# Kernel tuning notes

Hardware: AMD Instinct MI355X
Metric: run time of the kernel (lower is better)

## Reference

```python
import jax, jax.numpy as jnp
import numpy as np

N_QUBITS = 10
N_LAYERS = 4
DIM = 1 << N_QUBITS            # 1024
N3 = 3 * N_QUBITS              # params per rotation layer
N_PARAM = N3 * (N_LAYERS + 1)  # 150
BATCH = 8192

_C64 = jnp.complex64


def _rx(t):
    c = jnp.cos(t / 2).astype(_C64)
    s = jnp.sin(t / 2).astype(_C64)
    return jnp.stack([jnp.stack([c, -1j * s]), jnp.stack([-1j * s, c])])


def _ry(t):
    c = jnp.cos(t / 2).astype(_C64)
    s = jnp.sin(t / 2).astype(_C64)
    return jnp.stack([jnp.stack([c, -s]), jnp.stack([s, c])])


def _rz(t):
    e = jnp.exp(-1j * t.astype(_C64) / 2)
    z = jnp.zeros((), _C64)
    return jnp.stack([jnp.stack([e, z]), jnp.stack([z, jnp.conj(e)])])


def _apply1(state, gate, wire):
    """Apply a 2x2 gate to qubit `wire` of state [B, 2, ..., 2]."""
    axis = wire + 1  # axis 0 is batch
    s = jnp.moveaxis(state, axis, -1)
    s = jnp.einsum('ij,...j->...i', gate, s)
    return jnp.moveaxis(s, -1, axis)


def _cnot(state, ctrl, tgt):
    a, b = ctrl + 1, tgt + 1
    s = jnp.moveaxis(state, (a, b), (-2, -1))  # [..., ctrl, tgt]
    s = jnp.stack([s[..., 0, :], s[..., 1, ::-1]], axis=-2)
    return jnp.moveaxis(s, (-2, -1), (a, b))


def setup_inputs() -> dict:
    key = jax.random.key(0)
    k1, k2 = jax.random.split(key)
    x = jax.random.normal(k1, (BATCH, DIM), dtype=jnp.float32)
    he_std = (2.0 ** 0.5) * (5.0 ** -0.5)  # gain * 5^-0.5, w_mul with lrmul=1
    weight = jax.random.uniform(k2, (N_PARAM,), minval=0.0,
                                maxval=2.0 * np.pi, dtype=jnp.float32) * he_std
    return {"x": x, "weight": weight}


def reference(x, weight):
    # encoding layer: L2-normalize then cast to complex amplitudes
    norm = jnp.linalg.norm(x, axis=-1, keepdims=True)
    s = (x / jnp.maximum(norm, 1e-12)).astype(_C64)
    s = s.reshape((x.shape[0],) + (2,) * N_QUBITS)

    for l in range(N_LAYERS):
        w = weight[l * N3:(l + 1) * N3]
        # XYZ layer: Rx, then Ry, then Rz on every qubit
        for q in range(N_QUBITS):
            s = _apply1(s, _rx(w[q]), q)
        for q in range(N_QUBITS):
            s = _apply1(s, _ry(w[N_QUBITS + q]), q)
        for q in range(N_QUBITS):
            s = _apply1(s, _rz(w[2 * N_QUBITS + q]), q)
        # ring of CNOTs
        for q in range(N_QUBITS):
            s = _cnot(s, q, (q + 1) % N_QUBITS)

    # final YZY layer
    w = weight[N_LAYERS * N3:]
    for q in range(N_QUBITS):
        s = _apply1(s, _ry(w[q]), q)
    for q in range(N_QUBITS):
        s = _apply1(s, _rz(w[N_QUBITS + q]), q)
    for q in range(N_QUBITS):
        s = _apply1(s, _ry(w[2 * N_QUBITS + q]), q)

    return s.reshape(x.shape[0], 1, DIM).real
```

## Files before the change

### kernel.cpp

```cpp
#include <hip/hip_runtime.h>
#include <stdint.h>

typedef uint16_t u16;
typedef __attribute__((ext_vector_type(2))) float f32x2;
typedef __attribute__((ext_vector_type(4))) float f32x4;
typedef __attribute__((ext_vector_type(8))) short short8;
typedef __attribute__((ext_vector_type(4))) float float4v;
typedef __attribute__((ext_vector_type(4))) uint16_t u16x4;
typedef __attribute__((ext_vector_type(8))) uint16_t u16x8;

#define DIMQ 1024
#define BATCH 8192
#define KDIM 1024
#define NDIM 1024

#define RDL(v, l) __int_as_float(__builtin_amdgcn_readlane(__float_as_int(v), (l)))

__device__ __forceinline__ u16 f2bf(float f) {
  uint32_t u = __float_as_uint(f);
  u += 0x7fffu + ((u >> 16) & 1u);
  return (u16)(u >> 16);
}

template<int MASK>
__device__ __forceinline__ float lane_xor(float x) {
  if constexpr (MASK == 1)
    return __int_as_float(__builtin_amdgcn_update_dpp(0, __float_as_int(x), 0xB1, 0xF, 0xF, true));
  else if constexpr (MASK == 2)
    return __int_as_float(__builtin_amdgcn_update_dpp(0, __float_as_int(x), 0x4E, 0xF, 0xF, true));
  else if constexpr (MASK == 8)
    return __int_as_float(__builtin_amdgcn_update_dpp(0, __float_as_int(x), 0x128, 0xF, 0xF, true));
  else if constexpr (MASK == 4)
    return __int_as_float(__builtin_amdgcn_ds_swizzle(__float_as_int(x), 0x101F));
  else if constexpr (MASK == 16)
    return __int_as_float(__builtin_amdgcn_ds_swizzle(__float_as_int(x), 0x401F));
  else
    return __shfl_xor(x, 32, 64);
}

template<int MASK>
__device__ __forceinline__ void lane_gate8(float* ar, float* ai, int lane,
    float u00r, float u00i, float u01r, float u01i,
    float u10r, float u10i, float u11r, float u11i) {
  bool hi = (lane & MASK) != 0;
  float cmr = hi ? u11r : u00r, cmi = hi ? u11i : u00i;
  float cor = hi ? u10r : u01r, coi = hi ? u10i : u01i;
  float otr[8], oti[8];
#pragma unroll
  for (int r = 0; r < 8; ++r) otr[r] = lane_xor<MASK>(ar[r]);
#pragma unroll
  for (int r = 0; r < 8; ++r) oti[r] = lane_xor<MASK>(ai[r]);
#pragma unroll
  for (int k = 0; k < 4; ++k) {
    f32x2 A = {ar[2*k], ar[2*k+1]}, I = {ai[2*k], ai[2*k+1]};
    f32x2 R = {otr[2*k], otr[2*k+1]}, J = {oti[2*k], oti[2*k+1]};
    f32x2 nr = A*cmr - I*cmi + R*cor - J*coi;
    f32x2 ni = I*cmr + A*cmi + J*cor + R*coi;
    ar[2*k] = nr[0]; ar[2*k+1] = nr[1];
    ai[2*k] = ni[0]; ai[2*k+1] = ni[1];
  }
}

__device__ __forceinline__ void bfly2(f32x2 &a0r, f32x2 &a0i, f32x2 &a1r, f32x2 &a1i,
    float u00r, float u00i, float u01r, float u01i,
    float u10r, float u10i, float u11r, float u11i) {
  f32x2 t0r = a0r*u00r - a0i*u00i + a1r*u01r - a1i*u01i;
  f32x2 t0i = a0i*u00r + a0r*u00i + a1i*u01r + a1r*u01i;
  f32x2 t1r = a0r*u10r - a0i*u10i + a1r*u11r - a1i*u11i;
  f32x2 t1i = a0i*u10r + a0r*u10i + a1i*u11r + a1r*u11i;
  a0r = t0r; a0i = t0i; a1r = t1r; a1i = t1i;
}

__device__ inline void cmul2x2(float* O, const float* A, const float* B) {
  for (int r = 0; r < 2; ++r)
    for (int c = 0; c < 2; ++c) {
      float re = 0.f, im = 0.f;
      for (int j = 0; j < 2; ++j) {
        float ar = A[(r*2+j)*2], ai = A[(r*2+j)*2+1];
        float br = B[(j*2+c)*2], bi = B[(j*2+c)*2+1];
        re += ar*br - ai*bi;
        im += ar*bi + ai*br;
      }
      O[(r*2+c)*2]   = re;
      O[(r*2+c)*2+1] = im;
    }
}
__device__ inline void mk_rx(float* m, float t) {
  float s, c; sincosf(0.5f*t, &s, &c);
  m[0]=c; m[1]=0; m[2]=0; m[3]=-s; m[4]=0; m[5]=-s; m[6]=c; m[7]=0;
}
__device__ inline void mk_ry(float* m, float t) {
  float s, c; sincosf(0.5f*t, &s, &c);
  m[0]=c; m[1]=0; m[2]=-s; m[3]=0; m[4]=s; m[5]=0; m[6]=c; m[7]=0;
}
__device__ inline void mk_rz(float* m, float t) {
  float s, c; sincosf(0.5f*t, &s, &c);
  m[0]=c; m[1]=-s; m[2]=0; m[3]=0; m[4]=0; m[5]=0; m[6]=c; m[7]=s;
}

__device__ __forceinline__ int padi(int y) { return y + (y >> 4); }

__device__ __forceinline__ void do_stage(int gbase, float (&ar)[8], float (&ai)[8],
    f32x2* __restrict__ slab,
    const int (&idP0)[8], const int (&idP1)[8],
    int wbase, int lane, int h,
    float O0, float O1, float O2, float O3,
    float O4, float O5, float O6, float O7) {
  __syncthreads();
#pragma unroll
  for (int j = 0; j < 8; ++j) slab[wbase + j] = (f32x2){ar[j], ai[j]};
  __syncthreads();
  {
    int g = gbase + 6;
    float c0r = h ? RDL(O4,g) : RDL(O0,g), c0i = h ? RDL(O5,g) : RDL(O1,g);
    float c1r = h ? RDL(O6,g) : RDL(O2,g), c1i = h ? RDL(O7,g) : RDL(O3,g);
    f32x2 v0[8], v1[8];
#pragma unroll
    for (int j = 0; j < 8; ++j) {
      v0[j] = slab[idP0[j]];
      v1[j] = slab[idP1[j]];
    }
#pragma unroll
    for (int k = 0; k < 4; ++k) {
      f32x2 Vr0 = {v0[2*k][0], v0[2*k+1][0]}, Vi0 = {v0[2*k][1], v0[2*k+1][1]};
      f32x2 Vr1 = {v1[2*k][0], v1[2*k+1][0]}, Vi1 = {v1[2*k][1], v1[2*k+1][1]};
      f32x2 nr = Vr0*c0r - Vi0*c0i + Vr1*c1r - Vi1*c1i;
      f32x2 ni = Vi0*c0r + Vr0*c0i + Vi1*c1r + Vr1*c1i;
      ar[2*k] = nr[0]; ar[2*k+1] = nr[1];
      ai[2*k] = ni[0]; ai[2*k+1] = ni[1];
    }
  }
  { int g = gbase + 7;
    float u0r=RDL(O0,g),u0i=RDL(O1,g),u1r=RDL(O2,g),u1i=RDL(O3,g);
    float u2r=RDL(O4,g),u2i=RDL(O5,g),u3r=RDL(O6,g),u3i=RDL(O7,g);
    f32x2 a0r={ar[0],ar[1]}, a0i={ai[0],ai[1]}, a1r={ar[4],ar[5]}, a1i={ai[4],ai[5]};
    bfly2(a0r,a0i,a1r,a1i, u0r,u0i,u1r,u1i,u2r,u2i,u3r,u3i);
    ar[0]=a0r[0];ar[1]=a0r[1];ai[0]=a0i[0];ai[1]=a0i[1];
    ar[4]=a1r[0];ar[5]=a1r[1];ai[4]=a1i[0];ai[5]=a1i[1];
    f32x2 b0r={ar[2],ar[3]}, b0i={ai[2],ai[3]}, b1r={ar[6],ar[7]}, b1i={ai[6],ai[7]};
    bfly2(b0r,b0i,b1r,b1i, u0r,u0i,u1r,u1i,u2r,u2i,u3r,u3i);
    ar[2]=b0r[0];ar[3]=b0r[1];ai[2]=b0i[0];ai[3]=b0i[1];
    ar[6]=b1r[0];ar[7]=b1r[1];ai[6]=b1i[0];ai[7]=b1i[1];
  }
  { int g = gbase + 8;
    float u0r=RDL(O0,g),u0i=RDL(O1,g),u1r=RDL(O2,g),u1i=RDL(O3,g);
    float u2r=RDL(O4,g),u2i=RDL(O5,g),u3r=RDL(O6,g),u3i=RDL(O7,g);
    f32x2 a0r={ar[0],ar[1]}, a0i={ai[0],ai[1]}, a1r={ar[2],ar[3]}, a1i={ai[2],ai[3]};
    bfly2(a0r,a0i,a1r,a1i, u0r,u0i,u1r,u1i,u2r,u2i,u3r,u3i);
    ar[0]=a0r[0];ar[1]=a0r[1];ai[0]=a0i[0];ai[1]=a0i[1];
    ar[2]=a1r[0];ar[3]=a1r[1];ai[2]=a1i[0];ai[3]=a1i[1];
    f32x2 b0r={ar[4],ar[5]}, b0i={ai[4],ai[5]}, b1r={ar[6],ar[7]}, b1i={ai[6],ai[7]};
    bfly2(b0r,b0i,b1r,b1i, u0r,u0i,u1r,u1i,u2r,u2i,u3r,u3i);
    ar[4]=b0r[0];ar[5]=b0r[1];ai[4]=b0i[0];ai[5]=b0i[1];
    ar[6]=b1r[0];ar[7]=b1r[1];ai[6]=b1i[0];ai[7]=b1i[1];
  }
  { int g = gbase + 9;
    float u0r=RDL(O0,g),u0i=RDL(O1,g),u1r=RDL(O2,g),u1i=RDL(O3,g);
    float u2r=RDL(O4,g),u2i=RDL(O5,g),u3r=RDL(O6,g),u3i=RDL(O7,g);
    f32x2 a0r={ar[0],ar[2]}, a0i={ai[0],ai[2]}, a1r={ar[1],ar[3]}, a1i={ai[1],ai[3]};
    bfly2(a0r,a0i,a1r,a1i, u0r,u0i,u1r,u1i,u2r,u2i,u3r,u3i);
    ar[0]=a0r[0];ar[2]=a0r[1];ai[0]=a0i[0];ai[2]=a0i[1];
    ar[1]=a1r[0];ar[3]=a1r[1];ai[1]=a1i[0];ai[3]=a1i[1];
    f32x2 b0r={ar[4],ar[6]}, b0i={ai[4],ai[6]}, b1r={ar[5],ar[7]}, b1i={ai[5],ai[7]};
    bfly2(b0r,b0i,b1r,b1i, u0r,u0i,u1r,u1i,u2r,u2i,u3r,u3i);
    ar[4]=b0r[0];ar[6]=b0r[1];ai[4]=b0i[0];ai[6]=b0i[1];
    ar[5]=b1r[0];ar[7]=b1r[1];ai[5]=b1i[0];ai[7]=b1i[1];
  }
  { int g = gbase + 0; lane_gate8<32>(ar, ai, lane, RDL(O0,g),RDL(O1,g),RDL(O2,g),RDL(O3,g),RDL(O4,g),RDL(O5,g),RDL(O6,g),RDL(O7,g)); }
  { int g = gbase + 1; lane_gate8<16>(ar, ai, lane, RDL(O0,g),RDL(O1,g),RDL(O2,g),RDL(O3,g),RDL(O4,g),RDL(O5,g),RDL(O6,g),RDL(O7,g)); }
  { int g = gbase + 2; lane_gate8< 8>(ar, ai, lane, RDL(O0,g),RDL(O1,g),RDL(O2,g),RDL(O3,g),RDL(O4,g),RDL(O5,g),RDL(O6,g),RDL(O7,g)); }
  { int g = gbase + 3; lane_gate8< 4>(ar, ai, lane, RDL(O0,g),RDL(O1,g),RDL(O2,g),RDL(O3,g),RDL(O4,g),RDL(O5,g),RDL(O6,g),RDL(O7,g)); }
  { int g = gbase + 4; lane_gate8< 2>(ar, ai, lane, RDL(O0,g),RDL(O1,g),RDL(O2,g),RDL(O3,g),RDL(O4,g),RDL(O5,g),RDL(O6,g),RDL(O7,g)); }
  { int g = gbase + 5; lane_gate8< 1>(ar, ai, lane, RDL(O0,g),RDL(O1,g),RDL(O2,g),RDL(O3,g),RDL(O4,g),RDL(O5,g),RDL(O6,g),RDL(O7,g)); }
}

__global__ __launch_bounds__(256) void fused_front(const float* __restrict__ x,
                                                   const float* __restrict__ w,
                                                   u16* __restrict__ Abf,
                                                   u16* __restrict__ Bmat) {
  __shared__ f32x2 slab[2][1088];
  const int bid = blockIdx.x;
  const int lane = threadIdx.x & 63, wv = threadIdx.x >> 6;

  if (bid >= 512) {
    int base = (bid - 512) * 16 + wv * 4;
    for (int it = 0; it < 4; ++it) {
      int row = base + it;
      const float* xr = x + (size_t)row * DIMQ;
      float4v v[4];
      float ss = 0.f;
#pragma unroll
      for (int j = 0; j < 4; ++j) {
        v[j] = *(const float4v*)(xr + j*256 + lane*4);
        ss += v[j][0]*v[j][0] + v[j][1]*v[j][1] + v[j][2]*v[j][2] + v[j][3]*v[j][3];
      }
#pragma unroll
      for (int off = 32; off; off >>= 1) ss += __shfl_xor(ss, off, 64);
      float inv = 1.0f / fmaxf(sqrtf(ss), 1e-12f);
      u16* orow = Abf + (size_t)row * DIMQ;
#pragma unroll
      for (int j = 0; j < 4; ++j) {
        u16x4 o;
#pragma unroll
        for (int e = 0; e < 4; ++e) o[e] = f2bf(v[j][e] * inv);
        *(u16x4*)(orow + j*256 + lane*4) = o;
      }
    }
    return;
  }

  const int s = wv >> 1, h = wv & 1;
  const int d = bid * 2 + s;

  float O0, O1, O2, O3, O4, O5, O6, O7;
  {
    float A[8], B[8], C[8], T8[8], O[8];
    int t = lane;
    if (t < 50) {
      if (t < 10) {
        mk_ry(A, -w[120 + t]);
        mk_rz(B, -w[130 + t]);
        mk_ry(C, -w[140 + t]);
      } else {
        int sg = (t - 10) / 10, q = (t - 10) % 10, l = 3 - sg;
        mk_rx(A, -w[l*30 + q]);
        mk_ry(B, -w[l*30 + 10 + q]);
        mk_rz(C, -w[l*30 + 20 + q]);
      }
      cmul2x2(T8, A, B);
      cmul2x2(O, T8, C);
    } else {
#pragma unroll
      for (int j = 0; j < 8; ++j) O[j] = 0.f;
    }
    O0=O[0]; O1=O[1]; O2=O[2]; O3=O[3]; O4=O[4]; O5=O[5]; O6=O[6]; O7=O[7];
  }

  int idP0[8], idP1[8];
  int s8;
  {
    int yy = 8;
#pragma unroll
    for (int qq = 0; qq < 9; ++qq) yy ^= ((yy >> (9 - qq)) & 1) << (8 - qq);
    yy ^= (yy & 1) << 9;
    s8 = yy;
  }
#pragma unroll
  for (int j = 0; j < 8; ++j) {
    int xx = (lane << 4) + j;
    int yy = xx;
#pragma unroll
    for (int qq = 0; qq < 9; ++qq) yy ^= ((yy >> (9 - qq)) & 1) << (8 - qq);
    yy ^= (yy & 1) << 9;
    idP0[j] = padi(yy);
    idP1[j] = padi(yy ^ s8);
  }
  const int wbase = lane * 17 + h * 8;

  float ar[8], ai[8];
  {
    float fr = 1.0f, fi = 0.0f;
#pragma unroll
    for (int p = 4; p <= 9; ++p) {
      const int q = 9 - p;
      int c = (d >> p) & 1;
      float a0r = c ? RDL(O2,q) : RDL(O0,q), a0i = c ? RDL(O3,q) : RDL(O1,q);
      float a1r = c ? RDL(O6,q) : RDL(O4,q), a1i = c ? RDL(O7,q) : RDL(O5,q);
      bool hb = (lane >> (p - 4)) & 1;
      float gr = hb ? a1r : a0r, gi = hb ? a1i : a0i;
      float nr = fr*gr - fi*gi, ni = fr*gi + fi*gr;
      fr = nr; fi = ni;
    }
    {
      int c = (d >> 3) & 1;
      float a0r = c ? RDL(O2,6) : RDL(O0,6), a0i = c ? RDL(O3,6) : RDL(O1,6);
      float a1r = c ? RDL(O6,6) : RDL(O4,6), a1i = c ? RDL(O7,6) : RDL(O5,6);
      float gr = h ? a1r : a0r, gi = h ? a1i : a0i;
      float nr = fr*gr - fi*gi, ni = fr*gi + fi*gr;
      fr = nr; fi = ni;
    }
    float t2r[2], t2i[2], t1r[2], t1i[2], t0r[2], t0i[2];
    {
      int c = (d >> 2) & 1;
      t2r[0] = c ? RDL(O2,7) : RDL(O0,7); t2i[0] = c ? RDL(O3,7) : RDL(O1,7);
      t2r[1] = c ? RDL(O6,7) : RDL(O4,7); t2i[1] = c ? RDL(O7,7) : RDL(O5,7);
    }
    {
      int c = (d >> 1) & 1;
      t1r[0] = c ? RDL(O2,8) : RDL(O0,8); t1i[0] = c ? RDL(O3,8) : RDL(O1,8);
      t1r[1] = c ? RDL(O6,8) : RDL(O4,8); t1i[1] = c ? RDL(O7,8) : RDL(O5,8);
    }
    {
      int c = d & 1;
      t0r[0] = c ? RDL(O2,9) : RDL(O0,9); t0i[0] = c ? RDL(O3,9) : RDL(O1,9);
      t0r[1] = c ? RDL(O6,9) : RDL(O4,9); t0i[1] = c ? RDL(O7,9) : RDL(O5,9);
    }
    float m21r[4], m21i[4];
#pragma unroll
    for (int b2 = 0; b2 < 2; ++b2)
#pragma unroll
      for (int b1 = 0; b1 < 2; ++b1) {
        m21r[b2*2+b1] = t2r[b2]*t1r[b1] - t2i[b2]*t1i[b1];
        m21i[b2*2+b1] = t2r[b2]*t1i[b1] + t2i[b2]*t1r[b1];
      }
#pragma unroll
    for (int j = 0; j < 8; ++j) {
      int hi2 = j >> 1;
      int b0 = j & 1;
      float wr = m21r[hi2]*t0r[b0] - m21i[hi2]*t0i[b0];
      float wi = m21r[hi2]*t0i[b0] + m21i[hi2]*t0r[b0];
      ar[j] = fr*wr - fi*wi;
      ai[j] = fr*wi + fi*wr;
    }
  }

#pragma clang loop unroll(disable)
  for (int stage = 1; stage < 5; ++stage)
    do_stage(stage*10, ar, ai, slab[s], idP0, idP1, wbase, lane, h,
             O0,O1,O2,O3,O4,O5,O6,O7);

  u16x8 o;
#pragma unroll
  for (int j = 0; j < 8; ++j) o[j] = f2bf(ar[j]);
  *(u16x8*)(Bmat + (size_t)d * DIMQ + lane*16 + h*8) = o;
}

__global__ __launch_bounds__(512) void gemm_bt(const u16* __restrict__ A,
                                               const u16* __restrict__ Bm,
                                               float* __restrict__ C) {
  __shared__ u16 As[2][256*64];
  __shared__ u16 Bs[2][128*64];
  const int t = threadIdx.x, lane = t & 63, wave = t >> 6;
  int bid = blockIdx.x;
  int nid = ((bid & 7) << 5) | (bid >> 3);
  const int bm = nid >> 3, bn = nid & 7;
  const size_t aBase = (size_t)bm * 256 * KDIM;
  const size_t bBase = (size_t)bn * 128 * KDIM;

  const int srow = t >> 3;
  const int scol = ((t & 7) ^ (srow & 7)) * 8;
  const int dstB = srow * 128 + (t & 7) * 16;

  const int wm = wave >> 2, wn = wave & 3;
  const int la = lane & 15;
  const int lkB = ((lane >> 4) * 16);
  const int rsw = (lane & 7) << 4;

  f32x4 acc[8][2];
#pragma unroll
  for (int m = 0; m < 8; ++m)
#pragma unroll
    for (int n = 0; n < 2; ++n) acc[m][n] = (f32x4){0.f, 0.f, 0.f, 0.f};

  auto stage = [&](int b, int kt) {
    int k0 = kt * 64;
#pragma unroll
    for (int j = 0; j < 4; ++j) {
      __builtin_amdgcn_global_load_lds(
          (const __attribute__((address_space(1))) void*)(A + aBase + (size_t)(j*64 + srow)*KDIM + k0 + scol),
          (__attribute__((address_space(3))) void*)((char*)&As[b][0] + j*8192 + dstB), 16, 0, 0);
    }
#pragma unroll
    for (int j = 0; j < 2; ++j) {
      __builtin_amdgcn_global_load_lds(
          (const __attribute__((address_space(1))) void*)(Bm + bBase + (size_t)(j*64 + srow)*KDIM + k0 + scol),
          (__attribute__((address_space(3))) void*)((char*)&Bs[b][0] + j*8192 + dstB), 16, 0, 0);
    }
  };

  stage(0, 0);
  __syncthreads();

  int cur = 0;
  for (int kt = 0; kt < 16; ++kt) {
    if (kt < 15) stage(cur ^ 1, kt + 1);
    short8 af[8][2], bf[2][2];
#pragma unroll
    for (int kk = 0; kk < 2; ++kk) {
#pragma unroll
      for (int m = 0; m < 8; ++m) {
        int row = wm*128 + m*16 + la;
        int byt = (row*128 + kk*64 + lkB) ^ rsw;
        af[m][kk] = *(const short8*)((char*)&As[cur][0] + byt);
      }
#pragma unroll
      for (int n = 0; n < 2; ++n) {
        int row = wn*32 + n*16 + la;
        int byt = (row*128 + kk*64 + lkB) ^ rsw;
        bf[n][kk] = *(const short8*)((char*)&Bs[cur][0] + byt);
      }
    }
    __builtin_amdgcn_s_setprio(1);
#pragma unroll
    for (int kk = 0; kk < 2; ++kk)
#pragma unroll
      for (int m = 0; m < 8; ++m)
#pragma unroll
        for (int n = 0; n < 2; ++n)
          acc[m][n] = __builtin_amdgcn_mfma_f32_16x16x32_bf16(af[m][kk], bf[n][kk], acc[m][n], 0, 0, 0);
    __builtin_amdgcn_s_setprio(0);
    __syncthreads();
    cur ^= 1;
  }

  int orow0 = bm*256 + wm*128 + (lane >> 4)*4;
  int ocol0 = bn*128 + wn*32 + la;
#pragma unroll
  for (int m = 0; m < 8; ++m)
#pragma unroll
    for (int n = 0; n < 2; ++n)
#pragma unroll
      for (int j = 0; j < 4; ++j)
        C[(size_t)(orow0 + m*16 + j)*NDIM + ocol0 + n*16] = acc[m][n][j];
}

extern "C" void kernel_launch(void* const* d_in, const int* in_sizes, int n_in,
                              void* d_out, int out_size, void* d_ws, size_t ws_size,
                              hipStream_t stream) {
  const float* x = (const float*)d_in[0];
  const float* w = (const float*)d_in[1];
  float* out = (float*)d_out;
  char* ws = (char*)d_ws;
  u16* Bmat = (u16*)(ws + 4096);
  u16* Abf  = (u16*)(ws + 4096 + 2*1024*1024);

  fused_front<<<1024, 256, 0, stream>>>(x, w, Abf, Bmat);
  gemm_bt<<<(BATCH/256)*(NDIM/128), 512, 0, stream>>>(Abf, Bmat, out);
}
```

Measured before the change: 56.09 us.

## Spread each basis column over four waves and fuse two shuffled qubit gates

The state-simulation part of the fused front kernel now assigns one basis column per block, using four waves with four amplitudes per lane instead of two columns per block with eight per lane. The two qubits that cross waves (gates 6 and 7) are combined into one Kronecker-product coefficient applied during the shared-memory gather, which reads four partners per amplitude. The grid grows to 1536 blocks to cover the extra simulation blocks alongside the normalization blocks. This lowers register pressure and raises parallelism, at the cost of more shared-memory reads per amplitude and more block-wide barriers in total.

```diff
diff --git a/kernel.cpp b/kernel.cpp
--- a/kernel.cpp
+++ b/kernel.cpp
@@ -39,19 +39,19 @@
 }
 
 template<int MASK>
-__device__ __forceinline__ void lane_gate8(float* ar, float* ai, int lane,
+__device__ __forceinline__ void lane_gate4(float* ar, float* ai, int lane,
     float u00r, float u00i, float u01r, float u01i,
     float u10r, float u10i, float u11r, float u11i) {
   bool hi = (lane & MASK) != 0;
   float cmr = hi ? u11r : u00r, cmi = hi ? u11i : u00i;
   float cor = hi ? u10r : u01r, coi = hi ? u10i : u01i;
-  float otr[8], oti[8];
-#pragma unroll
-  for (int r = 0; r < 8; ++r) otr[r] = lane_xor<MASK>(ar[r]);
-#pragma unroll
-  for (int r = 0; r < 8; ++r) oti[r] = lane_xor<MASK>(ai[r]);
-#pragma unroll
-  for (int k = 0; k < 4; ++k) {
+  float otr[4], oti[4];
+#pragma unroll
+  for (int r = 0; r < 4; ++r) otr[r] = lane_xor<MASK>(ar[r]);
+#pragma unroll
+  for (int r = 0; r < 4; ++r) oti[r] = lane_xor<MASK>(ai[r]);
+#pragma unroll
+  for (int k = 0; k < 2; ++k) {
     f32x2 A = {ar[2*k], ar[2*k+1]}, I = {ai[2*k], ai[2*k+1]};
     f32x2 R = {otr[2*k], otr[2*k+1]}, J = {oti[2*k], oti[2*k+1]};
     f32x2 nr = A*cmr - I*cmi + R*cor - J*coi;
@@ -100,90 +100,16 @@
 
 __device__ __forceinline__ int padi(int y) { return y + (y >> 4); }
 
-__device__ __forceinline__ void do_stage(int gbase, float (&ar)[8], float (&ai)[8],
-    f32x2* __restrict__ slab,
-    const int (&idP0)[8], const int (&idP1)[8],
-    int wbase, int lane, int h,
-    float O0, float O1, float O2, float O3,
-    float O4, float O5, float O6, float O7) {
-  __syncthreads();
-#pragma unroll
-  for (int j = 0; j < 8; ++j) slab[wbase + j] = (f32x2){ar[j], ai[j]};
-  __syncthreads();
-  {
-    int g = gbase + 6;
-    float c0r = h ? RDL(O4,g) : RDL(O0,g), c0i = h ? RDL(O5,g) : RDL(O1,g);
-    float c1r = h ? RDL(O6,g) : RDL(O2,g), c1i = h ? RDL(O7,g) : RDL(O3,g);
-    f32x2 v0[8], v1[8];
-#pragma unroll
-    for (int j = 0; j < 8; ++j) {
-      v0[j] = slab[idP0[j]];
-      v1[j] = slab[idP1[j]];
-    }
-#pragma unroll
-    for (int k = 0; k < 4; ++k) {
-      f32x2 Vr0 = {v0[2*k][0], v0[2*k+1][0]}, Vi0 = {v0[2*k][1], v0[2*k+1][1]};
-      f32x2 Vr1 = {v1[2*k][0], v1[2*k+1][0]}, Vi1 = {v1[2*k][1], v1[2*k+1][1]};
-      f32x2 nr = Vr0*c0r - Vi0*c0i + Vr1*c1r - Vi1*c1i;
-      f32x2 ni = Vi0*c0r + Vr0*c0i + Vi1*c1r + Vr1*c1i;
-      ar[2*k] = nr[0]; ar[2*k+1] = nr[1];
-      ai[2*k] = ni[0]; ai[2*k+1] = ni[1];
-    }
-  }
-  { int g = gbase + 7;
-    float u0r=RDL(O0,g),u0i=RDL(O1,g),u1r=RDL(O2,g),u1i=RDL(O3,g);
-    float u2r=RDL(O4,g),u2i=RDL(O5,g),u3r=RDL(O6,g),u3i=RDL(O7,g);
-    f32x2 a0r={ar[0],ar[1]}, a0i={ai[0],ai[1]}, a1r={ar[4],ar[5]}, a1i={ai[4],ai[5]};
-    bfly2(a0r,a0i,a1r,a1i, u0r,u0i,u1r,u1i,u2r,u2i,u3r,u3i);
-    ar[0]=a0r[0];ar[1]=a0r[1];ai[0]=a0i[0];ai[1]=a0i[1];
-    ar[4]=a1r[0];ar[5]=a1r[1];ai[4]=a1i[0];ai[5]=a1i[1];
-    f32x2 b0r={ar[2],ar[3]}, b0i={ai[2],ai[3]}, b1r={ar[6],ar[7]}, b1i={ai[6],ai[7]};
-    bfly2(b0r,b0i,b1r,b1i, u0r,u0i,u1r,u1i,u2r,u2i,u3r,u3i);
-    ar[2]=b0r[0];ar[3]=b0r[1];ai[2]=b0i[0];ai[3]=b0i[1];
-    ar[6]=b1r[0];ar[7]=b1r[1];ai[6]=b1i[0];ai[7]=b1i[1];
-  }
-  { int g = gbase + 8;
-    float u0r=RDL(O0,g),u0i=RDL(O1,g),u1r=RDL(O2,g),u1i=RDL(O3,g);
-    float u2r=RDL(O4,g),u2i=RDL(O5,g),u3r=RDL(O6,g),u3i=RDL(O7,g);
-    f32x2 a0r={ar[0],ar[1]}, a0i={ai[0],ai[1]}, a1r={ar[2],ar[3]}, a1i={ai[2],ai[3]};
-    bfly2(a0r,a0i,a1r,a1i, u0r,u0i,u1r,u1i,u2r,u2i,u3r,u3i);
-    ar[0]=a0r[0];ar[1]=a0r[1];ai[0]=a0i[0];ai[1]=a0i[1];
-    ar[2]=a1r[0];ar[3]=a1r[1];ai[2]=a1i[0];ai[3]=a1i[1];
-    f32x2 b0r={ar[4],ar[5]}, b0i={ai[4],ai[5]}, b1r={ar[6],ar[7]}, b1i={ai[6],ai[7]};
-    bfly2(b0r,b0i,b1r,b1i, u0r,u0i,u1r,u1i,u2r,u2i,u3r,u3i);
-    ar[4]=b0r[0];ar[5]=b0r[1];ai[4]=b0i[0];ai[5]=b0i[1];
-    ar[6]=b1r[0];ar[7]=b1r[1];ai[6]=b1i[0];ai[7]=b1i[1];
-  }
-  { int g = gbase + 9;
-    float u0r=RDL(O0,g),u0i=RDL(O1,g),u1r=RDL(O2,g),u1i=RDL(O3,g);
-    float u2r=RDL(O4,g),u2i=RDL(O5,g),u3r=RDL(O6,g),u3i=RDL(O7,g);
-    f32x2 a0r={ar[0],ar[2]}, a0i={ai[0],ai[2]}, a1r={ar[1],ar[3]}, a1i={ai[1],ai[3]};
-    bfly2(a0r,a0i,a1r,a1i, u0r,u0i,u1r,u1i,u2r,u2i,u3r,u3i);
-    ar[0]=a0r[0];ar[2]=a0r[1];ai[0]=a0i[0];ai[2]=a0i[1];
-    ar[1]=a1r[0];ar[3]=a1r[1];ai[1]=a1i[0];ai[3]=a1i[1];
-    f32x2 b0r={ar[4],ar[6]}, b0i={ai[4],ai[6]}, b1r={ar[5],ar[7]}, b1i={ai[5],ai[7]};
-    bfly2(b0r,b0i,b1r,b1i, u0r,u0i,u1r,u1i,u2r,u2i,u3r,u3i);
-    ar[4]=b0r[0];ar[6]=b0r[1];ai[4]=b0i[0];ai[6]=b0i[1];
-    ar[5]=b1r[0];ar[7]=b1r[1];ai[5]=b1i[0];ai[7]=b1i[1];
-  }
-  { int g = gbase + 0; lane_gate8<32>(ar, ai, lane, RDL(O0,g),RDL(O1,g),RDL(O2,g),RDL(O3,g),RDL(O4,g),RDL(O5,g),RDL(O6,g),RDL(O7,g)); }
-  { int g = gbase + 1; lane_gate8<16>(ar, ai, lane, RDL(O0,g),RDL(O1,g),RDL(O2,g),RDL(O3,g),RDL(O4,g),RDL(O5,g),RDL(O6,g),RDL(O7,g)); }
-  { int g = gbase + 2; lane_gate8< 8>(ar, ai, lane, RDL(O0,g),RDL(O1,g),RDL(O2,g),RDL(O3,g),RDL(O4,g),RDL(O5,g),RDL(O6,g),RDL(O7,g)); }
-  { int g = gbase + 3; lane_gate8< 4>(ar, ai, lane, RDL(O0,g),RDL(O1,g),RDL(O2,g),RDL(O3,g),RDL(O4,g),RDL(O5,g),RDL(O6,g),RDL(O7,g)); }
-  { int g = gbase + 4; lane_gate8< 2>(ar, ai, lane, RDL(O0,g),RDL(O1,g),RDL(O2,g),RDL(O3,g),RDL(O4,g),RDL(O5,g),RDL(O6,g),RDL(O7,g)); }
-  { int g = gbase + 5; lane_gate8< 1>(ar, ai, lane, RDL(O0,g),RDL(O1,g),RDL(O2,g),RDL(O3,g),RDL(O4,g),RDL(O5,g),RDL(O6,g),RDL(O7,g)); }
-}
-
 __global__ __launch_bounds__(256) void fused_front(const float* __restrict__ x,
                                                    const float* __restrict__ w,
                                                    u16* __restrict__ Abf,
                                                    u16* __restrict__ Bmat) {
-  __shared__ f32x2 slab[2][1088];
+  __shared__ f32x2 slab[1088];
   const int bid = blockIdx.x;
   const int lane = threadIdx.x & 63, wv = threadIdx.x >> 6;
 
-  if (bid >= 512) {
-    int base = (bid - 512) * 16 + wv * 4;
+  if (bid >= 1024) {
+    int base = (bid - 1024) * 16 + wv * 4;
     for (int it = 0; it < 4; ++it) {
       int row = base + it;
       const float* xr = x + (size_t)row * DIMQ;
@@ -209,8 +135,7 @@
     return;
   }
 
-  const int s = wv >> 1, h = wv & 1;
-  const int d = bid * 2 + s;
+  const int d = bid;
 
   float O0, O1, O2, O3, O4, O5, O6, O7;
   {
@@ -236,28 +161,23 @@
     O0=O[0]; O1=O[1]; O2=O[2]; O3=O[3]; O4=O[4]; O5=O[5]; O6=O[6]; O7=O[7];
   }
 
-  int idP0[8], idP1[8];
-  int s8;
+  int idP[4][4];
   {
-    int yy = 8;
-#pragma unroll
-    for (int qq = 0; qq < 9; ++qq) yy ^= ((yy >> (9 - qq)) & 1) << (8 - qq);
-    yy ^= (yy & 1) << 9;
-    s8 = yy;
-  }
-#pragma unroll
-  for (int j = 0; j < 8; ++j) {
-    int xx = (lane << 4) + j;
-    int yy = xx;
-#pragma unroll
-    for (int qq = 0; qq < 9; ++qq) yy ^= ((yy >> (9 - qq)) & 1) << (8 - qq);
-    yy ^= (yy & 1) << 9;
-    idP0[j] = padi(yy);
-    idP1[j] = padi(yy ^ s8);
-  }
-  const int wbase = lane * 17 + h * 8;
-
-  float ar[8], ai[8];
+    const int T[4] = {0, 519, 527, 8};
+#pragma unroll
+    for (int j = 0; j < 4; ++j) {
+      int xx = (lane << 4) | j;
+      int yy = xx;
+#pragma unroll
+      for (int qq = 0; qq < 9; ++qq) yy ^= ((yy >> (9 - qq)) & 1) << (8 - qq);
+      yy ^= (yy & 1) << 9;
+#pragma unroll
+      for (int wp = 0; wp < 4; ++wp) idP[j][wp] = padi(yy ^ T[wp]);
+    }
+  }
+  const int wbase = lane * 17 + wv * 4;
+
+  float ar[4], ai[4];
   {
     float fr = 1.0f, fi = 0.0f;
 #pragma unroll
@@ -275,16 +195,21 @@
       int c = (d >> 3) & 1;
       float a0r = c ? RDL(O2,6) : RDL(O0,6), a0i = c ? RDL(O3,6) : RDL(O1,6);
       float a1r = c ? RDL(O6,6) : RDL(O4,6), a1i = c ? RDL(O7,6) : RDL(O5,6);
-      float gr = h ? a1r : a0r, gi = h ? a1i : a0i;
+      bool hb = (wv >> 1) & 1;
+      float gr = hb ? a1r : a0r, gi = hb ? a1i : a0i;
       float nr = fr*gr - fi*gi, ni = fr*gi + fi*gr;
       fr = nr; fi = ni;
     }
-    float t2r[2], t2i[2], t1r[2], t1i[2], t0r[2], t0i[2];
     {
       int c = (d >> 2) & 1;
-      t2r[0] = c ? RDL(O2,7) : RDL(O0,7); t2i[0] = c ? RDL(O3,7) : RDL(O1,7);
-      t2r[1] = c ? RDL(O6,7) : RDL(O4,7); t2i[1] = c ? RDL(O7,7) : RDL(O5,7);
-    }
+      float a0r = c ? RDL(O2,7) : RDL(O0,7), a0i = c ? RDL(O3,7) : RDL(O1,7);
+      float a1r = c ? RDL(O6,7) : RDL(O4,7), a1i = c ? RDL(O7,7) : RDL(O5,7);
+      bool hb = wv & 1;
+      float gr = hb ? a1r : a0r, gi = hb ? a1i : a0i;
+      float nr = fr*gr - fi*gi, ni = fr*gi + fi*gr;
+      fr = nr; fi = ni;
+    }
+    float t1r[2], t1i[2], t0r[2], t0i[2];
     {
       int c = (d >> 1) & 1;
       t1r[0] = c ? RDL(O2,8) : RDL(O0,8); t1i[0] = c ? RDL(O3,8) : RDL(O1,8);
@@ -295,34 +220,85 @@
       t0r[0] = c ? RDL(O2,9) : RDL(O0,9); t0i[0] = c ? RDL(O3,9) : RDL(O1,9);
       t0r[1] = c ? RDL(O6,9) : RDL(O4,9); t0i[1] = c ? RDL(O7,9) : RDL(O5,9);
     }
-    float m21r[4], m21i[4];
-#pragma unroll
-    for (int b2 = 0; b2 < 2; ++b2)
-#pragma unroll
-      for (int b1 = 0; b1 < 2; ++b1) {
-        m21r[b2*2+b1] = t2r[b2]*t1r[b1] - t2i[b2]*t1i[b1];
-        m21i[b2*2+b1] = t2r[b2]*t1i[b1] + t2i[b2]*t1r[b1];
-      }
-#pragma unroll
-    for (int j = 0; j < 8; ++j) {
-      int hi2 = j >> 1;
-      int b0 = j & 1;
-      float wr = m21r[hi2]*t0r[b0] - m21i[hi2]*t0i[b0];
-      float wi = m21r[hi2]*t0i[b0] + m21i[hi2]*t0r[b0];
-      ar[j] = fr*wr - fi*wi;
-      ai[j] = fr*wi + fi*wr;
+#pragma unroll
+    for (int j = 0; j < 4; ++j) {
+      int b1 = j >> 1, b0 = j & 1;
+      float mr = t1r[b1]*t0r[b0] - t1i[b1]*t0i[b0];
+      float mi = t1r[b1]*t0i[b0] + t1i[b1]*t0r[b0];
+      ar[j] = fr*mr - fi*mi;
+      ai[j] = fr*mi + fi*mr;
     }
   }
 
 #pragma clang loop unroll(disable)
-  for (int stage = 1; stage < 5; ++stage)
-    do_stage(stage*10, ar, ai, slab[s], idP0, idP1, wbase, lane, h,
-             O0,O1,O2,O3,O4,O5,O6,O7);
-
-  u16x8 o;
-#pragma unroll
-  for (int j = 0; j < 8; ++j) o[j] = f2bf(ar[j]);
-  *(u16x8*)(Bmat + (size_t)d * DIMQ + lane*16 + h*8) = o;
+  for (int stage = 1; stage < 5; ++stage) {
+    const int gbase = stage * 10;
+    __syncthreads();
+#pragma unroll
+    for (int j = 0; j < 4; ++j) slab[wbase + j] = (f32x2){ar[j], ai[j]};
+    __syncthreads();
+    {
+      int g6 = gbase + 6, g7 = gbase + 7;
+      bool r6 = (wv >> 1) & 1, r7 = wv & 1;
+      float u6r[2], u6i[2], u7r[2], u7i[2];
+      u6r[0] = r6 ? RDL(O4,g6) : RDL(O0,g6); u6i[0] = r6 ? RDL(O5,g6) : RDL(O1,g6);
+      u6r[1] = r6 ? RDL(O6,g6) : RDL(O2,g6); u6i[1] = r6 ? RDL(O7,g6) : RDL(O3,g6);
+      u7r[0] = r7 ? RDL(O4,g7) : RDL(O0,g7); u7i[0] = r7 ? RDL(O5,g7) : RDL(O1,g7);
+      u7r[1] = r7 ? RDL(O6,g7) : RDL(O2,g7); u7i[1] = r7 ? RDL(O7,g7) : RDL(O3,g7);
+      float Kr[4], Ki[4];
+#pragma unroll
+      for (int wp = 0; wp < 4; ++wp) {
+        int c6 = wp >> 1, c7 = wp & 1;
+        Kr[wp] = u6r[c6]*u7r[c7] - u6i[c6]*u7i[c7];
+        Ki[wp] = u6r[c6]*u7i[c7] + u6i[c6]*u7r[c7];
+      }
+      f32x2 v[4][4];
+#pragma unroll
+      for (int j = 0; j < 4; ++j)
+#pragma unroll
+        for (int wp = 0; wp < 4; ++wp) v[j][wp] = slab[idP[j][wp]];
+#pragma unroll
+      for (int k = 0; k < 2; ++k) {
+        f32x2 nr = {0.f, 0.f}, ni = {0.f, 0.f};
+#pragma unroll
+        for (int wp = 0; wp < 4; ++wp) {
+          f32x2 Vr = {v[2*k][wp][0], v[2*k+1][wp][0]};
+          f32x2 Vi = {v[2*k][wp][1], v[2*k+1][wp][1]};
+          nr += Vr*Kr[wp] - Vi*Ki[wp];
+          ni += Vi*Kr[wp] + Vr*Ki[wp];
+        }
+        ar[2*k] = nr[0]; ar[2*k+1] = nr[1];
+        ai[2*k] = ni[0]; ai[2*k+1] = ni[1];
+      }
+    }
+    { int g = gbase + 8;
+      float u0r=RDL(O0,g),u0i=RDL(O1,g),u1r=RDL(O2,g),u1i=RDL(O3,g);
+      float u2r=RDL(O4,g),u2i=RDL(O5,g),u3r=RDL(O6,g),u3i=RDL(O7,g);
+      f32x2 a0r={ar[0],ar[1]}, a0i={ai[0],ai[1]}, a1r={ar[2],ar[3]}, a1i={ai[2],ai[3]};
+      bfly2(a0r,a0i,a1r,a1i, u0r,u0i,u1r,u1i,u2r,u2i,u3r,u3i);
+      ar[0]=a0r[0];ar[1]=a0r[1];ai[0]=a0i[0];ai[1]=a0i[1];
+      ar[2]=a1r[0];ar[3]=a1r[1];ai[2]=a1i[0];ai[3]=a1i[1];
+    }
+    { int g = gbase + 9;
+      float u0r=RDL(O0,g),u0i=RDL(O1,g),u1r=RDL(O2,g),u1i=RDL(O3,g);
+      float u2r=RDL(O4,g),u2i=RDL(O5,g),u3r=RDL(O6,g),u3i=RDL(O7,g);
+      f32x2 a0r={ar[0],ar[2]}, a0i={ai[0],ai[2]}, a1r={ar[1],ar[3]}, a1i={ai[1],ai[3]};
+      bfly2(a0r,a0i,a1r,a1i, u0r,u0i,u1r,u1i,u2r,u2i,u3r,u3i);
+      ar[0]=a0r[0];ar[2]=a0r[1];ai[0]=a0i[0];ai[2]=a0i[1];
+      ar[1]=a1r[0];ar[3]=a1r[1];ai[1]=a1i[0];ai[3]=a1i[1];
+    }
+    { int g = gbase + 0; lane_gate4<32>(ar, ai, lane, RDL(O0,g),RDL(O1,g),RDL(O2,g),RDL(O3,g),RDL(O4,g),RDL(O5,g),RDL(O6,g),RDL(O7,g)); }
+    { int g = gbase + 1; lane_gate4<16>(ar, ai, lane, RDL(O0,g),RDL(O1,g),RDL(O2,g),RDL(O3,g),RDL(O4,g),RDL(O5,g),RDL(O6,g),RDL(O7,g)); }
+    { int g = gbase + 2; lane_gate4< 8>(ar, ai, lane, RDL(O0,g),RDL(O1,g),RDL(O2,g),RDL(O3,g),RDL(O4,g),RDL(O5,g),RDL(O6,g),RDL(O7,g)); }
+    { int g = gbase + 3; lane_gate4< 4>(ar, ai, lane, RDL(O0,g),RDL(O1,g),RDL(O2,g),RDL(O3,g),RDL(O4,g),RDL(O5,g),RDL(O6,g),RDL(O7,g)); }
+    { int g = gbase + 4; lane_gate4< 2>(ar, ai, lane, RDL(O0,g),RDL(O1,g),RDL(O2,g),RDL(O3,g),RDL(O4,g),RDL(O5,g),RDL(O6,g),RDL(O7,g)); }
+    { int g = gbase + 5; lane_gate4< 1>(ar, ai, lane, RDL(O0,g),RDL(O1,g),RDL(O2,g),RDL(O3,g),RDL(O4,g),RDL(O5,g),RDL(O6,g),RDL(O7,g)); }
+  }
+
+  u16x4 o;
+#pragma unroll
+  for (int j = 0; j < 4; ++j) o[j] = f2bf(ar[j]);
+  *(u16x4*)(Bmat + (size_t)d * DIMQ + lane*16 + wv*4) = o;
 }
 
 __global__ __launch_bounds__(512) void gemm_bt(const u16* __restrict__ A,
@@ -424,6 +400,6 @@
   u16* Bmat = (u16*)(ws + 4096);
   u16* Abf  = (u16*)(ws + 4096 + 2*1024*1024);
 
-  fused_front<<<1024, 256, 0, stream>>>(x, w, Abf, Bmat);
+  fused_front<<<1536, 256, 0, stream>>>(x, w, Abf, Bmat);
   gemm_bt<<<(BATCH/256)*(NDIM/128), 512, 0, stream>>>(Abf, Bmat, out);
 }
```

Result: slower. 58.76 us (+4.8%).
